# Performance work log

Measured on AMD Instinct MI355X. Metric: run time of the kernel, lower is better.

The kernel has to match this reference:

```python
import jax, jax.numpy as jnp
import numpy as np

VOCAB, EMB, HID, KSZ, VSZ = 10000, 512, 1024, 128, 128
N, T_ENC, T_DEC = 64, 500, 200


def lstm_cell(x, h, c, W_ih, W_hh, b_ih, b_hh):
    # PyTorch LSTMCell gate order: i, f, g, o
    gates = x @ W_ih.T + b_ih + h @ W_hh.T + b_hh
    i, f, g, o = jnp.split(gates, 4, axis=-1)
    c_new = jax.nn.sigmoid(f) * c + jax.nn.sigmoid(i) * jnp.tanh(g)
    h_new = jax.nn.sigmoid(o) * jnp.tanh(c_new)
    return h_new, c_new


def setup_inputs() -> dict:
    key = jax.random.key(0)
    ks = jax.random.split(key, 16)
    s = 0.02
    emb_table = jax.random.normal(ks[0], (VOCAB, EMB), jnp.float32) * s
    emb_table = emb_table.at[0].set(0.0)  # padding_idx=0
    inp = {
        "key": jax.random.normal(ks[1], (N, T_ENC, KSZ), jnp.float32),
        "value": jax.random.normal(ks[2], (N, T_ENC, VSZ), jnp.float32),
        "src_lens": jax.random.randint(ks[3], (N,), 1, T_ENC + 1),
        "text": jax.random.randint(ks[4], (N, T_DEC), 0, VOCAB),
        "emb_table": emb_table,
        "W_ih1": jax.random.normal(ks[5], (4 * HID, EMB + VSZ), jnp.float32) * s,
        "W_hh1": jax.random.normal(ks[6], (4 * HID, HID), jnp.float32) * s,
        "b_ih1": jnp.zeros((4 * HID,), jnp.float32),
        "b_hh1": jnp.zeros((4 * HID,), jnp.float32),
        "W_ih2": jax.random.normal(ks[7], (4 * KSZ, HID), jnp.float32) * s,
        "W_hh2": jax.random.normal(ks[8], (4 * KSZ, KSZ), jnp.float32) * s,
        "b_ih2": jnp.zeros((4 * KSZ,), jnp.float32),
        "b_hh2": jnp.zeros((4 * KSZ,), jnp.float32),
        "W_out": jax.random.normal(ks[9], (VOCAB, KSZ + VSZ), jnp.float32) * s,
        "b_out": jnp.zeros((VOCAB,), jnp.float32),
    }
    return inp


def reference(key, value, src_lens, text, emb_table, W_ih1, W_hh1, b_ih1, b_hh1,
              W_ih2, W_hh2, b_ih2, b_hh2, W_out, b_out):
    n, t_enc = key.shape[0], key.shape[1]
    # attention mask over encoder steps: True where position >= src_len
    mask = jnp.arange(t_enc)[None, :] >= src_lens[:, None]  # (N, T_enc)
    embeddings = emb_table[text]  # (N, T_dec, EMB) teacher forcing

    def step(carry, x_emb):
        h1, c1, h2, c2 = carry
        # attention: query = h2 (output of 2nd LSTMCell)
        energy = jnp.einsum('ntk,nk->nt', key, h2)
        energy = jnp.where(mask, -1e9, energy)
        att = jax.nn.softmax(energy, axis=1)
        ctx = jnp.einsum('nt,ntv->nv', att, value)
        inp = jnp.concatenate([x_emb, ctx], axis=1)
        h1, c1 = lstm_cell(inp, h1, c1, W_ih1, W_hh1, b_ih1, b_hh1)
        h2, c2 = lstm_cell(h1, h2, c2, W_ih2, W_hh2, b_ih2, b_hh2)
        logits = jnp.concatenate([h2, ctx], axis=1) @ W_out.T + b_out
        return (h1, c1, h2, c2), logits

    init = (jnp.zeros((n, W_hh1.shape[1])), jnp.zeros((n, W_hh1.shape[1])),
            jnp.zeros((n, W_hh2.shape[1])), jnp.zeros((n, W_hh2.shape[1])))
    _, preds = jax.lax.scan(step, init, jnp.swapaxes(embeddings, 0, 1))
    return jnp.swapaxes(preds, 0, 1)  # (N, T_dec, VOCAB)
```

## Files before the change

kernel.cpp:

```cpp
#include <hip/hip_runtime.h>
#include <hip/hip_bf16.h>
#include <math.h>


#define NB    64
#define TENC  500
#define TDEC  200
#define EMBD  512
#define HID   1024
#define KSZ   128
#define VSZ   128
#define VOCAB 10000
#define K1    1664
#define K2    1152
#define NWG   256
#define NTH   512

typedef __bf16 bf16x8 __attribute__((ext_vector_type(8)));
typedef float f32x4 __attribute__((ext_vector_type(4)));
typedef unsigned long long u64;
#define MFMA16(a, b, c) __builtin_amdgcn_mfma_f32_16x16x32_bf16((a), (b), (c), 0, 0, 0)

constexpr size_t OFF_BAR   = 0;
constexpr size_t OFF_BS1   = 4096;
constexpr size_t OFF_BS2   = 20480;
constexpr size_t OFF_W2    = 22528;
constexpr size_t OFF_H2C   = 1202176;
constexpr size_t OFF_W1    = 7755776;
constexpr size_t OFF_WOUT  = 21387264;
constexpr size_t OFF_XEMB  = 26507264;
constexpr size_t OFF_H1R   = 39614464;
constexpr size_t OFF_CTXR  = 65959936;
constexpr size_t BIG_END   = 69253120;
constexpr size_t OFF_KEYBF = 69253120;
constexpr size_t OFF_VALBF = 77445120;
constexpr size_t KV_END    = 85637120;

__device__ __forceinline__ float sigm(float x) { return 1.0f / (1.0f + __expf(-x)); }
__device__ __forceinline__ float ftanh(float x) {
  float ax = fabsf(x);
  float e = __expf(2.0f * ax);
  float tv = 1.0f - 2.0f / (e + 1.0f);
  return copysignf(tv, x);
}
__device__ __forceinline__ float bf2f(unsigned u) { return __uint_as_float(u << 16); }
__device__ __forceinline__ bf16x8 ldfrag(const __hip_bfloat16* p) {
  return *reinterpret_cast<const bf16x8*>(p);
}
__device__ __forceinline__ bf16x8 ldfrag_nt(const __hip_bfloat16* p) {
  union { u64 u[2]; bf16x8 v; } r;
  r.u[0] = __builtin_nontemporal_load((const u64*)p);
  r.u[1] = __builtin_nontemporal_load((const u64*)(p + 4));
  return r.v;
}
__device__ __forceinline__ void st_u32_sys(void* p, unsigned v) {
  __hip_atomic_store((unsigned*)p, v, __ATOMIC_RELAXED, __HIP_MEMORY_SCOPE_AGENT);
}
__device__ __forceinline__ void st_u16_sys(void* p, unsigned short v) {
  __hip_atomic_store((unsigned short*)p, v, __ATOMIC_RELAXED, __HIP_MEMORY_SCOPE_AGENT);
}
__device__ __forceinline__ unsigned ld_u32_sys(const void* p) {
  return __hip_atomic_load((const unsigned*)p, __ATOMIC_RELAXED, __HIP_MEMORY_SCOPE_AGENT);
}
__device__ __forceinline__ unsigned pack2bf(float a, float b) {
  __hip_bfloat16 ha = __float2bfloat16(a), hb = __float2bfloat16(b);
  unsigned short ua = *(unsigned short*)&ha, ub = *(unsigned short*)&hb;
  return (unsigned)ua | ((unsigned)ub << 16);
}
__device__ __forceinline__ unsigned short f2bfu(float x) {
  __hip_bfloat16 h = __float2bfloat16(x);
  return *(unsigned short*)&h;
}

__global__ __launch_bounds__(256) void k_prep_w1(const float* __restrict__ Wih1,
                                                 const float* __restrict__ Whh1,
                                                 const float* __restrict__ bih1,
                                                 const float* __restrict__ bhh1,
                                                 __hip_bfloat16* __restrict__ W1bf,
                                                 float* __restrict__ bsum1) {
  int r = blockIdx.x;
  const float* wi = Wih1 + (size_t)r * 640;
  const float* wh = Whh1 + (size_t)r * 1024;
  for (int k = threadIdx.x; k < K1; k += 256)
    W1bf[(size_t)r * K1 + k] = __float2bfloat16(k < 640 ? wi[k] : wh[k - 640]);
  if (threadIdx.x == 0) bsum1[r] = bih1[r] + bhh1[r];
}

__global__ __launch_bounds__(256) void k_prep_w2(const float* __restrict__ Wih2,
                                                 const float* __restrict__ Whh2,
                                                 const float* __restrict__ bih2,
                                                 const float* __restrict__ bhh2,
                                                 __hip_bfloat16* __restrict__ W2bf,
                                                 float* __restrict__ bsum2) {
  int r = blockIdx.x;
  for (int k = threadIdx.x; k < K2; k += 256)
    W2bf[(size_t)r * K2 + k] =
        __float2bfloat16(k < 1024 ? Wih2[(size_t)r * 1024 + k]
                                  : Whh2[(size_t)r * 128 + k - 1024]);
  if (threadIdx.x == 0) bsum2[r] = bih2[r] + bhh2[r];
}

__global__ __launch_bounds__(256) void k_prep_wout(const float* __restrict__ Wout,
                                                   __hip_bfloat16* __restrict__ Woutbf) {
  int r0 = blockIdx.x * 16;
  for (int idx = threadIdx.x; idx < 16 * 256; idx += 256) {
    int r = r0 + (idx >> 8), k = idx & 255;
    Woutbf[(size_t)r * 256 + k] = __float2bfloat16(Wout[(size_t)r * 256 + k]);
  }
}

__global__ __launch_bounds__(256) void k_gather(const int* __restrict__ text,
                                                const float* __restrict__ emb,
                                                __hip_bfloat16* __restrict__ xembbf) {
  int t = blockIdx.x;
  __shared__ int tok[NB];
  if (threadIdx.x < NB) tok[threadIdx.x] = text[threadIdx.x * TDEC + t];
  __syncthreads();
  for (int idx = threadIdx.x; idx < NB * EMBD; idx += 256) {
    int n = idx >> 9, k = idx & 511;
    xembbf[((size_t)t * NB + n) * EMBD + k] =
        __float2bfloat16(emb[(size_t)tok[n] * EMBD + k]);
  }
}

__global__ __launch_bounds__(256) void k_prep_kv(const float* __restrict__ key,
                                                 const float* __restrict__ value,
                                                 __hip_bfloat16* __restrict__ keybf,
                                                 __hip_bfloat16* __restrict__ valbf) {
  int gsz = gridDim.x * 256;
  for (size_t i = blockIdx.x * 256 + threadIdx.x; i < (size_t)NB * TENC * KSZ; i += gsz) {
    keybf[i] = __float2bfloat16(key[i]);
    valbf[i] = __float2bfloat16(value[i]);
  }
}

__device__ __forceinline__ void gbar(unsigned* cnt, int ep, int wg, bool inv) {
  asm volatile("s_waitcnt vmcnt(0)" ::: "memory");
  __syncthreads();
  int tid = threadIdx.x;
  if (tid == 0) {
    if (inv)
      __hip_atomic_fetch_add(&cnt[(wg & 7) << 4], 1u, __ATOMIC_ACQ_REL,
                             __HIP_MEMORY_SCOPE_AGENT);
    else
      __hip_atomic_fetch_add(&cnt[(wg & 7) << 4], 1u, __ATOMIC_RELAXED,
                             __HIP_MEMORY_SCOPE_AGENT);
  }
  if (tid < 64) {
    unsigned need = (unsigned)ep * 16u;
    for (;;) {
      unsigned v = __hip_atomic_load(&cnt[(tid & 7) << 4], __ATOMIC_RELAXED,
                                     __HIP_MEMORY_SCOPE_AGENT);
      if (__all((int)(v >= need))) break;
      __builtin_amdgcn_s_sleep(1);
    }
    if (inv) {
      unsigned vv = __hip_atomic_load(&cnt[(tid & 7) << 4], __ATOMIC_ACQUIRE,
                                      __HIP_MEMORY_SCOPE_AGENT);
      (void)vv;
    }
  }
  __syncthreads();
}

struct LA {
  const float* key;
  const float* value;
  const int* slen;
  const __hip_bfloat16* keybf;
  const __hip_bfloat16* valbf;
  int kv;
  int big;
  const __hip_bfloat16* W1bf;
  const __hip_bfloat16* W2bf;
  const __hip_bfloat16* Woutbf;
  const __hip_bfloat16* xembbf;
  const float* bsum1;
  const float* bsum2;
  const float* bout;
  float* out;
  __hip_bfloat16* h1r;
  __hip_bfloat16* ctxr;
  __hip_bfloat16* h2cbf;
  __hip_bfloat16* pbuf;
  unsigned* ms;
  unsigned* flags;
  unsigned* bar_cnt;
};

__global__ __launch_bounds__(NTH) void k_loop(LA a) {
  const int wg = blockIdx.x, tid = threadIdx.x;

  __shared__ float bs1l[8][4];
  __shared__ unsigned short stmp[512];
  __shared__ __align__(16) char smem[33792];
  float* part = (float*)smem;
  float* gl   = (float*)(smem + 8192);
  float* partL = (float*)smem;
  float* glL   = (float*)(smem + 4096);
  float* h2s  = (float*)smem;
  float* e_l  = (float*)(smem + 2048);
  float* red  = (float*)(smem + 4096);
  float* ctxp = (float*)(smem + 6144);

  if (wg >= 128) {
    int o0 = wg - 128;
    int lane = tid & 63, w4 = tid >> 6;
    int ln15 = lane & 15, lg = lane >> 4, ko = lg * 8;
    for (int t = 0; t < TDEC; ++t) {
      if (tid < 64) {
        unsigned need = (3u * (unsigned)t + 3u) * 16u;
        for (;;) {
          unsigned v = __hip_atomic_load(&a.bar_cnt[(tid & 7) << 4],
                                         __ATOMIC_RELAXED, __HIP_MEMORY_SCOPE_AGENT);
          if (__all((int)(v >= need))) break;
          __builtin_amdgcn_s_sleep(8);
        }
      }
      __syncthreads();
      if (w4 < 4) {
        const __hip_bfloat16* ap =
            a.h2cbf + ((size_t)t * NB + w4 * 16 + ln15) * 256;
        bf16x8 afr[8];
        #pragma unroll
        for (int kk = 0; kk < 8; ++kk) afr[kk] = ldfrag(ap + kk * 32 + ko);
        for (int sub = 0; sub < 2; ++sub) {
          int o = o0 + sub * 128;
          if (o >= 157) break;
          int c0 = o * 64;
          #pragma unroll
          for (int s = 0; s < 4; ++s) {
            int c = c0 + s * 16 + ln15;
            bool ok = c < VOCAB;
            const __hip_bfloat16* bp = a.Woutbf + (size_t)c * 256;
            f32x4 acc = {0.f, 0.f, 0.f, 0.f};
            #pragma unroll
            for (int kk = 0; kk < 8; ++kk) {
              bf16x8 bv = ok ? ldfrag_nt(bp + kk * 32 + ko) : bf16x8{};
              acc = MFMA16(afr[kk], bv, acc);
            }
            if (ok) {
              float bb = a.bout[c];
              #pragma unroll
              for (int reg = 0; reg < 4; ++reg) {
                int nrow = w4 * 16 + 4 * lg + reg;
                __builtin_nontemporal_store(
                    acc[reg] + bb, &a.out[((size_t)nrow * TDEC + t) * VOCAB + c]);
              }
            }
          }
        }
      }
    }
    return;
  }

  const int lane = tid & 63, wid = tid >> 6;
  const int ln15 = lane & 15, lg = lane >> 4, ko = lg * 8;
  const int bg = wid & 3, kh = wid >> 2;
  const int d0 = wg * 8;
  const bool inv = (a.big == 0);
  const bool isMain = (wg < 64);
  const int n = wg & 63;
  const int len = a.slen[n];

  float creg0 = 0.f;
  float creg2 = 0.f;

  const __hip_bfloat16 *wb0, *wb1;
  {
    int g = ln15 & 3, s = ln15 >> 2;
    wb0 = a.W1bf + (size_t)(g * 1024 + d0 + 0 + s) * K1;
    wb1 = a.W1bf + (size_t)(g * 1024 + d0 + 4 + s) * K1;
  }
  const __hip_bfloat16* w2p = a.W2bf + (size_t)((ln15 & 3) * 128 + wg) * K2;
  const int nA = bg * 16 + ln15;

  if (tid < 32) bs1l[tid >> 2][tid & 3] = a.bsum1[(tid & 3) * 1024 + d0 + (tid >> 2)];
  if (isMain) {
    int v = tid & 127, ph = tid >> 7;
    float acc = 0.f;
    if (a.kv) {
      const unsigned short* vb = (const unsigned short*)a.valbf;
      for (int p = ph; p < len; p += 4)
        acc += bf2f(vb[((size_t)n * TENC + p) * VSZ + v]);
    } else {
      for (int p = ph; p < len; p += 4)
        acc += a.value[((size_t)n * TENC + p) * VSZ + v];
    }
    ctxp[ph * 128 + v] = acc;
    __syncthreads();
    if (tid < 64) {
      int vp = tid;
      float invl = 1.f / (float)len;
      float c0 = (ctxp[0 * 128 + 2 * vp] + ctxp[1 * 128 + 2 * vp] +
                  ctxp[2 * 128 + 2 * vp] + ctxp[3 * 128 + 2 * vp]) * invl;
      float c1 = (ctxp[0 * 128 + 2 * vp + 1] + ctxp[1 * 128 + 2 * vp + 1] +
                  ctxp[2 * 128 + 2 * vp + 1] + ctxp[3 * 128 + 2 * vp + 1]) * invl;
      unsigned pk = pack2bf(c0, c1);
      st_u32_sys(a.ctxr + (size_t)n * 128 + 2 * vp, pk);
      st_u32_sys(&a.h2cbf[((size_t)0 * NB + n) * 256 + 128 + 2 * vp], pk);
    }
  }
  int ep = 0;
  gbar(a.bar_cnt, ++ep, wg, inv);

  for (int t = 0; t < TDEC; ++t) {
    const __hip_bfloat16 *h1c, *ctxc;
    __hip_bfloat16 *h1n, *ctxn;
    if (a.big) {
      h1c = a.h1r + (size_t)t * 65536;
      h1n = a.h1r + (size_t)(t + 1) * 65536;
      ctxc = a.ctxr + (size_t)t * 8192;
      ctxn = a.ctxr + (size_t)(t + 1) * 8192;
    } else {
      h1c = a.h1r + (size_t)(t & 1) * 65536;
      h1n = a.h1r + (size_t)((t + 1) & 1) * 65536;
      ctxc = a.ctxr;
      ctxn = a.ctxr;
    }

    {
      const __hip_bfloat16* ax = a.xembbf + ((size_t)t * NB + nA) * EMBD;
      const __hip_bfloat16* ac = ctxc + nA * 128;
      const __hip_bfloat16* ah = h1c + nA * 1024;
      f32x4 q0 = {0, 0, 0, 0}, q1 = {0, 0, 0, 0};
      if (kh == 0) {
        #pragma unroll
        for (int s = 0; s < 16; ++s) {
          bf16x8 av = ldfrag(ax + s * 32 + ko);
          int o = s * 32 + ko;
          q0 = MFMA16(av, ldfrag(wb0 + o), q0);
          q1 = MFMA16(av, ldfrag(wb1 + o), q1);
        }
        #pragma unroll
        for (int s = 0; s < 4; ++s) {
          bf16x8 av = ldfrag(ac + s * 32 + ko);
          int o = 512 + s * 32 + ko;
          q0 = MFMA16(av, ldfrag(wb0 + o), q0);
          q1 = MFMA16(av, ldfrag(wb1 + o), q1);
        }
        #pragma unroll
        for (int s = 0; s < 6; ++s) {
          bf16x8 av = ldfrag(ah + s * 32 + ko);
          int o = 640 + s * 32 + ko;
          q0 = MFMA16(av, ldfrag(wb0 + o), q0);
          q1 = MFMA16(av, ldfrag(wb1 + o), q1);
        }
      } else {
        #pragma unroll
        for (int s = 0; s < 26; ++s) {
          bf16x8 av = ldfrag(ah + 192 + s * 32 + ko);
          int o = 832 + s * 32 + ko;
          q0 = MFMA16(av, ldfrag(wb0 + o), q0);
          q1 = MFMA16(av, ldfrag(wb1 + o), q1);
        }
      }
      if (kh == 1) {
        *(f32x4*)&part[(((bg * 2 + 0) * 64) + lane) * 4] = q0;
        *(f32x4*)&part[(((bg * 2 + 1) * 64) + lane) * 4] = q1;
      }
      __syncthreads();
      if (kh == 0) {
        q0 += *(f32x4*)&part[(((bg * 2 + 0) * 64) + lane) * 4];
        q1 += *(f32x4*)&part[(((bg * 2 + 1) * 64) + lane) * 4];
        #pragma unroll
        for (int r = 0; r < 4; ++r) {
          gl[((bg * 2 + 0) * 16 + (lg * 4 + r)) * 16 + ln15] = q0[r];
          gl[((bg * 2 + 1) * 16 + (lg * 4 + r)) * 16 + ln15] = q1[r];
        }
      }
      __syncthreads();
      {
        int nn = tid >> 3, dp = tid & 7;
        int bgg = nn >> 4, ii = nn & 15;
        int f = dp >> 2, s = dp & 3;
        float4 gA = *(float4*)&gl[(((bgg * 2 + f) * 16) + ii) * 16 + s * 4];
        float I = sigm(gA.x + bs1l[dp][0]);
        float F = sigm(gA.y + bs1l[dp][1]);
        float G = ftanh(gA.z + bs1l[dp][2]);
        float O = sigm(gA.w + bs1l[dp][3]);
        float cv = F * creg0 + I * G;
        creg0 = cv;
        stmp[nn * 8 + dp] = f2bfu(O * ftanh(cv));
      }
      __syncthreads();
      if (tid < 256) {
        int n3 = tid >> 2, e = tid & 3;
        unsigned pk = (unsigned)stmp[n3 * 8 + e * 2] |
                      ((unsigned)stmp[n3 * 8 + e * 2 + 1] << 16);
        st_u32_sys(h1n + n3 * 1024 + d0 + e * 2, pk);
      }
    }
    gbar(a.bar_cnt, ++ep, wg, inv);

    {
      const __hip_bfloat16* ah = h1n + nA * 1024;
      f32x4 q = {0.f, 0.f, 0.f, 0.f};
      if (kh == 0) {
        #pragma unroll
        for (int s = 0; s < 18; ++s)
          q = MFMA16(ldfrag(ah + s * 32 + ko), ldfrag(w2p + s * 32 + ko), q);
      } else {
        #pragma unroll
        for (int s = 0; s < 14; ++s)
          q = MFMA16(ldfrag(ah + 576 + s * 32 + ko), ldfrag(w2p + 576 + s * 32 + ko), q);
        if (t > 0) {
          const __hip_bfloat16* hp = a.h2cbf + ((size_t)(t - 1) * NB + nA) * 256;
          #pragma unroll
          for (int s = 0; s < 4; ++s)
            q = MFMA16(ldfrag(hp + s * 32 + ko), ldfrag(w2p + 1024 + s * 32 + ko), q);
        }
      }
      if (kh == 1) *(f32x4*)&partL[(bg * 64 + lane) * 4] = q;
      __syncthreads();
      if (kh == 0) {
        q += *(f32x4*)&partL[(bg * 64 + lane) * 4];
        #pragma unroll
        for (int r = 0; r < 4; ++r)
          glL[(bg * 16 + lg * 4 + r) * 16 + ln15] = q[r];
      }
      __syncthreads();
      if (tid < 64) {
        int n2 = tid;
        float4 g4 = *(float4*)&glL[n2 * 16];
        float I = sigm(g4.x + a.bsum2[wg]);
        float F = sigm(g4.y + a.bsum2[128 + wg]);
        float G = ftanh(g4.z + a.bsum2[256 + wg]);
        float O = sigm(g4.w + a.bsum2[384 + wg]);
        float cv = F * creg2 + I * G;
        creg2 = cv;
        st_u16_sys((unsigned short*)a.h2cbf + ((size_t)t * NB + n2) * 256 + wg,
                   f2bfu(O * ftanh(cv)));
      }
    }
    gbar(a.bar_cnt, ++ep, wg, inv);

    if (t < TDEC - 1) {
      if (tid < 64) {
        unsigned u = *(const unsigned*)((const unsigned short*)a.h2cbf +
                                        ((size_t)t * NB + n) * 256 + 2 * tid);
        h2s[2 * tid] = bf2f(u & 0xffffu);
        h2s[2 * tid + 1] = bf2f(u >> 16);
      }
      __syncthreads();
      const int base = isMain ? 0 : 250;
      const int lim = isMain ? (a.big ? (len < 250 ? len : 250) : len) : len;
      int p = base + tid;
      float e = -1e30f;
      if (tid < 250 + (isMain ? 6 : 0) && p < lim) {
        float s = 0.f;
        if (a.kv) {
          const uint4* kr = (const uint4*)(a.keybf + ((size_t)n * TENC + p) * KSZ);
          #pragma unroll
          for (int kk = 0; kk < 16; ++kk) {
            uint4 u = kr[kk];
            const float* hh = &h2s[kk * 8];
            s += bf2f(u.x & 0xffffu) * hh[0] + bf2f(u.x >> 16) * hh[1]
               + bf2f(u.y & 0xffffu) * hh[2] + bf2f(u.y >> 16) * hh[3]
               + bf2f(u.z & 0xffffu) * hh[4] + bf2f(u.z >> 16) * hh[5]
               + bf2f(u.w & 0xffffu) * hh[6] + bf2f(u.w >> 16) * hh[7];
          }
        } else {
          const float4* kr = (const float4*)(a.key + ((size_t)n * TENC + p) * KSZ);
          #pragma unroll 8
          for (int kk = 0; kk < 32; ++kk) {
            float4 u = kr[kk];
            const float* hh = &h2s[kk * 4];
            s += u.x * hh[0] + u.y * hh[1] + u.z * hh[2] + u.w * hh[3];
          }
        }
        e = s;
      }
      red[tid] = e;
      __syncthreads();
      for (int s2 = 256; s2 > 0; s2 >>= 1) {
        if (tid < s2) red[tid] = fmaxf(red[tid], red[tid + s2]);
        __syncthreads();
      }
      float mA = red[0];
      __syncthreads();
      bool act = (tid < 250 + (isMain ? 6 : 0)) && (base + tid < lim);
      float ex = act ? __expf(e - mA) : 0.f;
      e_l[tid] = ex;
      red[tid] = ex;
      __syncthreads();
      for (int s2 = 256; s2 > 0; s2 >>= 1) {
        if (tid < s2) red[tid] += red[tid + s2];
        __syncthreads();
      }
      float SA = red[0];
      {
        int w = tid >> 6, ln = tid & 63;
        float a0 = 0.f, a1 = 0.f;
        if (a.kv) {
          const unsigned short* vb = (const unsigned short*)a.valbf;
          for (int p2 = base + w; p2 < lim; p2 += 8) {
            unsigned u = *(const unsigned*)(vb + ((size_t)n * TENC + p2) * VSZ + 2 * ln);
            float ew = e_l[p2 - base];
            a0 += ew * bf2f(u & 0xffffu);
            a1 += ew * bf2f(u >> 16);
          }
        } else {
          for (int p2 = base + w; p2 < lim; p2 += 8) {
            float2 vv = *(const float2*)(a.value + ((size_t)n * TENC + p2) * VSZ + 2 * ln);
            float ew = e_l[p2 - base];
            a0 += ew * vv.x;
            a1 += ew * vv.y;
          }
        }
        ctxp[w * 128 + 2 * ln] = a0;
        ctxp[w * 128 + 2 * ln + 1] = a1;
      }
      __syncthreads();
      if (!isMain) {
        if (tid < 64) {
          int vp = tid;
          float p0 = 0.f, p1 = 0.f;
          #pragma unroll
          for (int w2 = 0; w2 < 8; ++w2) {
            p0 += ctxp[w2 * 128 + 2 * vp];
            p1 += ctxp[w2 * 128 + 2 * vp + 1];
          }
          st_u32_sys(a.pbuf + n * 128 + 2 * vp, pack2bf(p0, p1));
        }
        if (tid == 0) {
          st_u32_sys(a.ms + n * 2, __float_as_uint(mA));
          st_u32_sys(a.ms + n * 2 + 1, __float_as_uint(SA));
        }
        asm volatile("s_waitcnt vmcnt(0)" ::: "memory");
        __syncthreads();
        if (tid == 0) st_u32_sys(&a.flags[n], (unsigned)(t + 1));
      } else {
        if (a.big && tid == 0) {
          while (__hip_atomic_load(&a.flags[n], __ATOMIC_RELAXED,
                                   __HIP_MEMORY_SCOPE_AGENT) < (unsigned)(t + 1))
            __builtin_amdgcn_s_sleep(2);
        }
        __syncthreads();
        if (tid < 64) {
          int vp = tid;
          float PA0 = 0.f, PA1 = 0.f;
          #pragma unroll
          for (int w2 = 0; w2 < 8; ++w2) {
            PA0 += ctxp[w2 * 128 + 2 * vp];
            PA1 += ctxp[w2 * 128 + 2 * vp + 1];
          }
          float c0, c1;
          if (a.big) {
            float mB = __uint_as_float(ld_u32_sys(a.ms + n * 2));
            float SB = __uint_as_float(ld_u32_sys(a.ms + n * 2 + 1));
            unsigned pbu = ld_u32_sys(a.pbuf + n * 128 + 2 * vp);
            float m2 = fmaxf(mA, mB);
            float fA = __expf(mA - m2), fB = __expf(mB - m2);
            float ivs = 1.f / (SA * fA + SB * fB);
            c0 = (PA0 * fA + bf2f(pbu & 0xffffu) * fB) * ivs;
            c1 = (PA1 * fA + bf2f(pbu >> 16) * fB) * ivs;
          } else {
            float ivs = 1.f / SA;
            c0 = PA0 * ivs;
            c1 = PA1 * ivs;
          }
          unsigned pk = pack2bf(c0, c1);
          st_u32_sys(ctxn + (size_t)n * 128 + 2 * vp, pk);
          st_u32_sys(&a.h2cbf[((size_t)(t + 1) * NB + n) * 256 + 128 + 2 * vp], pk);
        }
      }
    }
    gbar(a.bar_cnt, ++ep, wg, inv);
  }
}

extern "C" void kernel_launch(void* const* d_in, const int* in_sizes, int n_in,
                              void* d_out, int out_size, void* d_ws, size_t ws_size,
                              hipStream_t stream) {
  (void)in_sizes; (void)n_in; (void)out_size;
  const float* key   = (const float*)d_in[0];
  const float* value = (const float*)d_in[1];
  const int*   slen  = (const int*)d_in[2];
  const int*   text  = (const int*)d_in[3];
  const float* emb   = (const float*)d_in[4];
  const float* Wih1  = (const float*)d_in[5];
  const float* Whh1  = (const float*)d_in[6];
  const float* bih1  = (const float*)d_in[7];
  const float* bhh1  = (const float*)d_in[8];
  const float* Wih2  = (const float*)d_in[9];
  const float* Whh2  = (const float*)d_in[10];
  const float* bih2  = (const float*)d_in[11];
  const float* bhh2  = (const float*)d_in[12];
  const float* Wout  = (const float*)d_in[13];
  const float* bout  = (const float*)d_in[14];
  float* out = (float*)d_out;
  char* ws = (char*)d_ws;

  int big = (ws_size >= BIG_END) ? 1 : 0;
  int kv  = (ws_size >= KV_END) ? 1 : 0;

  __hip_bfloat16* W1bf   = (__hip_bfloat16*)(ws + OFF_W1);
  __hip_bfloat16* W2bf   = (__hip_bfloat16*)(ws + OFF_W2);
  __hip_bfloat16* Woutbf = (__hip_bfloat16*)(ws + OFF_WOUT);
  __hip_bfloat16* xembbf = (__hip_bfloat16*)(ws + OFF_XEMB);
  __hip_bfloat16* h2cbf  = (__hip_bfloat16*)(ws + OFF_H2C);
  float* bsum1 = (float*)(ws + OFF_BS1);
  float* bsum2 = (float*)(ws + OFF_BS2);
  __hip_bfloat16* keybf = (__hip_bfloat16*)(ws + OFF_KEYBF);
  __hip_bfloat16* valbf = (__hip_bfloat16*)(ws + OFF_VALBF);

  hipMemsetAsync(ws, 0, 4096, stream);
  hipMemsetAsync(ws + OFF_H1R, 0, 262144, stream);
  k_prep_w1<<<4096, 256, 0, stream>>>(Wih1, Whh1, bih1, bhh1, W1bf, bsum1);
  k_prep_w2<<<512, 256, 0, stream>>>(Wih2, Whh2, bih2, bhh2, W2bf, bsum2);
  k_prep_wout<<<625, 256, 0, stream>>>(Wout, Woutbf);
  k_gather<<<TDEC, 256, 0, stream>>>(text, emb, xembbf);
  if (kv) k_prep_kv<<<2048, 256, 0, stream>>>(key, value, keybf, valbf);

  LA la;
  la.key = key; la.value = value; la.slen = slen;
  la.keybf = keybf; la.valbf = valbf; la.kv = kv; la.big = big;
  la.W1bf = W1bf; la.W2bf = W2bf; la.Woutbf = Woutbf; la.xembbf = xembbf;
  la.bsum1 = bsum1; la.bsum2 = bsum2; la.bout = bout; la.out = out;
  la.h1r = (__hip_bfloat16*)(ws + OFF_H1R);
  la.ctxr = (__hip_bfloat16*)(ws + OFF_CTXR);
  la.h2cbf = h2cbf;
  la.pbuf = (__hip_bfloat16*)(ws + OFF_CTXR) + (size_t)200 * 8192;
  la.ms = (unsigned*)(ws + 2048);
  la.flags = (unsigned*)(ws + 2560);
  la.bar_cnt = (unsigned*)(ws + OFF_BAR);

  void* args[] = {&la};
  hipLaunchCooperativeKernel((void*)k_loop, dim3(NWG), dim3(NTH), args, 0, stream);
}
```

Measured before the change: 9.366 ms.

## Fuse LSTM2 into per-batch attention workgroups and drop a grid barrier

Moves the second LSTM cell out of a grid-distributed MFMA stage. Each of the 64 main workgroups now computes all 512 gates for its own batch row, using a transposed bf16 W2 and scalar dot products, and keeps h2/c2 in shared memory. This removes one grid-wide barrier per decoder step. The helper workgroups that handle the second half of the attention now wait on a per-row flag instead. In exchange, every main workgroup re-reads the full W2 matrix each step and does the gate math without tensor cores.

```diff
diff --git a/kernel.cpp b/kernel.cpp
--- a/kernel.cpp
+++ b/kernel.cpp
@@ -86,17 +86,19 @@
   if (threadIdx.x == 0) bsum1[r] = bih1[r] + bhh1[r];
 }
 
-__global__ __launch_bounds__(256) void k_prep_w2(const float* __restrict__ Wih2,
-                                                 const float* __restrict__ Whh2,
-                                                 const float* __restrict__ bih2,
-                                                 const float* __restrict__ bhh2,
-                                                 __hip_bfloat16* __restrict__ W2bf,
-                                                 float* __restrict__ bsum2) {
+__global__ __launch_bounds__(256) void k_prep_w2t(const float* __restrict__ Wih2,
+                                                  const float* __restrict__ Whh2,
+                                                  const float* __restrict__ bih2,
+                                                  const float* __restrict__ bhh2,
+                                                  __hip_bfloat16* __restrict__ W2T,
+                                                  float* __restrict__ bsum2) {
   int r = blockIdx.x;
-  for (int k = threadIdx.x; k < K2; k += 256)
-    W2bf[(size_t)r * K2 + k] =
-        __float2bfloat16(k < 1024 ? Wih2[(size_t)r * 1024 + k]
-                                  : Whh2[(size_t)r * 128 + k - 1024]);
+  for (int idx = threadIdx.x; idx < K2; idx += 256) {
+    int kb = idx >> 3, j = idx & 7;
+    float v = (idx < 1024) ? Wih2[(size_t)r * 1024 + idx]
+                           : Whh2[(size_t)r * 128 + idx - 1024];
+    W2T[((size_t)(kb * 512 + r)) * 8 + j] = __float2bfloat16(v);
+  }
   if (threadIdx.x == 0) bsum2[r] = bih2[r] + bhh2[r];
 }
 
@@ -172,7 +174,7 @@
   int kv;
   int big;
   const __hip_bfloat16* W1bf;
-  const __hip_bfloat16* W2bf;
+  const __hip_bfloat16* W2T;
   const __hip_bfloat16* Woutbf;
   const __hip_bfloat16* xembbf;
   const float* bsum1;
@@ -184,7 +186,8 @@
   __hip_bfloat16* h2cbf;
   __hip_bfloat16* pbuf;
   unsigned* ms;
-  unsigned* flags;
+  unsigned* pflag;
+  unsigned* hflag;
   unsigned* bar_cnt;
 };
 
@@ -193,15 +196,17 @@
 
   __shared__ float bs1l[8][4];
   __shared__ unsigned short stmp[512];
+  __shared__ float h2st[128];
+  __shared__ float c2st[128];
   __shared__ __align__(16) char smem[33792];
   float* part = (float*)smem;
   float* gl   = (float*)(smem + 8192);
-  float* partL = (float*)smem;
-  float* glL   = (float*)(smem + 4096);
-  float* h2s  = (float*)smem;
-  float* e_l  = (float*)(smem + 2048);
-  float* red  = (float*)(smem + 4096);
-  float* ctxp = (float*)(smem + 6144);
+  float* h1s  = (float*)smem;
+  float* g2   = (float*)(smem + 4096);
+  float* e_l  = (float*)(smem + 6144);
+  float* red  = (float*)(smem + 8192);
+  float* ctxp = (float*)(smem + 10240);
+  float* h2s  = (float*)(smem + 14336);
 
   if (wg >= 128) {
     int o0 = wg - 128;
@@ -209,7 +214,7 @@
     int ln15 = lane & 15, lg = lane >> 4, ko = lg * 8;
     for (int t = 0; t < TDEC; ++t) {
       if (tid < 64) {
-        unsigned need = (3u * (unsigned)t + 3u) * 16u;
+        unsigned need = (2u * (unsigned)t + 3u) * 16u;
         for (;;) {
           unsigned v = __hip_atomic_load(&a.bar_cnt[(tid & 7) << 4],
                                          __ATOMIC_RELAXED, __HIP_MEMORY_SCOPE_AGENT);
@@ -265,7 +270,6 @@
   const int len = a.slen[n];
 
   float creg0 = 0.f;
-  float creg2 = 0.f;
 
   const __hip_bfloat16 *wb0, *wb1;
   {
@@ -273,10 +277,10 @@
     wb0 = a.W1bf + (size_t)(g * 1024 + d0 + 0 + s) * K1;
     wb1 = a.W1bf + (size_t)(g * 1024 + d0 + 4 + s) * K1;
   }
-  const __hip_bfloat16* w2p = a.W2bf + (size_t)((ln15 & 3) * 128 + wg) * K2;
   const int nA = bg * 16 + ln15;
 
   if (tid < 32) bs1l[tid >> 2][tid & 3] = a.bsum1[(tid & 3) * 1024 + d0 + (tid >> 2)];
+  if (tid < 128) { h2st[tid] = 0.f; c2st[tid] = 0.f; }
   if (isMain) {
     int v = tid & 127, ph = tid >> 7;
     float acc = 0.f;
@@ -394,146 +398,115 @@
     }
     gbar(a.bar_cnt, ++ep, wg, inv);
 
-    {
-      const __hip_bfloat16* ah = h1n + nA * 1024;
-      f32x4 q = {0.f, 0.f, 0.f, 0.f};
-      if (kh == 0) {
-        #pragma unroll
-        for (int s = 0; s < 18; ++s)
-          q = MFMA16(ldfrag(ah + s * 32 + ko), ldfrag(w2p + s * 32 + ko), q);
-      } else {
-        #pragma unroll
-        for (int s = 0; s < 14; ++s)
-          q = MFMA16(ldfrag(ah + 576 + s * 32 + ko), ldfrag(w2p + 576 + s * 32 + ko), q);
-        if (t > 0) {
-          const __hip_bfloat16* hp = a.h2cbf + ((size_t)(t - 1) * NB + nA) * 256;
-          #pragma unroll
-          for (int s = 0; s < 4; ++s)
-            q = MFMA16(ldfrag(hp + s * 32 + ko), ldfrag(w2p + 1024 + s * 32 + ko), q);
-        }
-      }
-      if (kh == 1) *(f32x4*)&partL[(bg * 64 + lane) * 4] = q;
-      __syncthreads();
-      if (kh == 0) {
-        q += *(f32x4*)&partL[(bg * 64 + lane) * 4];
-        #pragma unroll
-        for (int r = 0; r < 4; ++r)
-          glL[(bg * 16 + lg * 4 + r) * 16 + ln15] = q[r];
-      }
-      __syncthreads();
-      if (tid < 64) {
-        int n2 = tid;
-        float4 g4 = *(float4*)&glL[n2 * 16];
-        float I = sigm(g4.x + a.bsum2[wg]);
-        float F = sigm(g4.y + a.bsum2[128 + wg]);
-        float G = ftanh(g4.z + a.bsum2[256 + wg]);
-        float O = sigm(g4.w + a.bsum2[384 + wg]);
-        float cv = F * creg2 + I * G;
-        creg2 = cv;
-        st_u16_sys((unsigned short*)a.h2cbf + ((size_t)t * NB + n2) * 256 + wg,
-                   f2bfu(O * ftanh(cv)));
-      }
-    }
-    gbar(a.bar_cnt, ++ep, wg, inv);
-
-    if (t < TDEC - 1) {
-      if (tid < 64) {
-        unsigned u = *(const unsigned*)((const unsigned short*)a.h2cbf +
-                                        ((size_t)t * NB + n) * 256 + 2 * tid);
-        h2s[2 * tid] = bf2f(u & 0xffffu);
-        h2s[2 * tid + 1] = bf2f(u >> 16);
-      }
-      __syncthreads();
-      const int base = isMain ? 0 : 250;
-      const int lim = isMain ? (a.big ? (len < 250 ? len : 250) : len) : len;
-      int p = base + tid;
-      float e = -1e30f;
-      if (tid < 250 + (isMain ? 6 : 0) && p < lim) {
-        float s = 0.f;
-        if (a.kv) {
-          const uint4* kr = (const uint4*)(a.keybf + ((size_t)n * TENC + p) * KSZ);
-          #pragma unroll
-          for (int kk = 0; kk < 16; ++kk) {
-            uint4 u = kr[kk];
-            const float* hh = &h2s[kk * 8];
-            s += bf2f(u.x & 0xffffu) * hh[0] + bf2f(u.x >> 16) * hh[1]
-               + bf2f(u.y & 0xffffu) * hh[2] + bf2f(u.y >> 16) * hh[3]
-               + bf2f(u.z & 0xffffu) * hh[4] + bf2f(u.z >> 16) * hh[5]
-               + bf2f(u.w & 0xffffu) * hh[6] + bf2f(u.w >> 16) * hh[7];
-          }
-        } else {
-          const float4* kr = (const float4*)(a.key + ((size_t)n * TENC + p) * KSZ);
-          #pragma unroll 8
-          for (int kk = 0; kk < 32; ++kk) {
-            float4 u = kr[kk];
-            const float* hh = &h2s[kk * 4];
-            s += u.x * hh[0] + u.y * hh[1] + u.z * hh[2] + u.w * hh[3];
-          }
-        }
-        e = s;
-      }
-      red[tid] = e;
-      __syncthreads();
-      for (int s2 = 256; s2 > 0; s2 >>= 1) {
-        if (tid < s2) red[tid] = fmaxf(red[tid], red[tid + s2]);
+    if (isMain) {
+      if (tid < 256) {
+        u64 u = *(const u64*)(h1n + (size_t)n * 1024 + tid * 4);
+        h1s[tid * 4 + 0] = bf2f((unsigned)(u & 0xffffu));
+        h1s[tid * 4 + 1] = bf2f((unsigned)((u >> 16) & 0xffffu));
+        h1s[tid * 4 + 2] = bf2f((unsigned)((u >> 32) & 0xffffu));
+        h1s[tid * 4 + 3] = bf2f((unsigned)(u >> 48));
+      }
+      __syncthreads();
+      {
+        float accg = 0.f;
+        #pragma unroll 8
+        for (int kb = 0; kb < 144; ++kb) {
+          uint4 wv = *(const uint4*)(a.W2T + ((size_t)kb * 512 + tid) * 8);
+          const float* in = (kb < 128) ? &h1s[kb * 8] : &h2st[(kb - 128) * 8];
+          accg += bf2f(wv.x & 0xffffu) * in[0] + bf2f(wv.x >> 16) * in[1]
+                + bf2f(wv.y & 0xffffu) * in[2] + bf2f(wv.y >> 16) * in[3]
+                + bf2f(wv.z & 0xffffu) * in[4] + bf2f(wv.z >> 16) * in[5]
+                + bf2f(wv.w & 0xffffu) * in[6] + bf2f(wv.w >> 16) * in[7];
+        }
+        g2[tid] = accg;
+      }
+      __syncthreads();
+      if (tid < 128) {
+        int d = tid;
+        float I = sigm(g2[d] + a.bsum2[d]);
+        float F = sigm(g2[128 + d] + a.bsum2[128 + d]);
+        float G = ftanh(g2[256 + d] + a.bsum2[256 + d]);
+        float O = sigm(g2[384 + d] + a.bsum2[384 + d]);
+        float cv = F * c2st[d] + I * G;
+        c2st[d] = cv;
+        float h = O * ftanh(cv);
+        h2st[d] = h;
+        st_u16_sys((unsigned short*)a.h2cbf + ((size_t)t * NB + n) * 256 + d,
+                   f2bfu(h));
+      }
+      asm volatile("s_waitcnt vmcnt(0)" ::: "memory");
+      __syncthreads();
+      if (tid == 0) st_u32_sys(&a.hflag[n], (unsigned)(t + 1));
+
+      if (t < TDEC - 1) {
+        const int lim = a.big ? (len < 250 ? len : 250) : len;
+        float e = -1e30f;
+        if (tid < 256 && tid < lim) {
+          float s = 0.f;
+          if (a.kv) {
+            const uint4* kr = (const uint4*)(a.keybf + ((size_t)n * TENC + tid) * KSZ);
+            #pragma unroll
+            for (int kk = 0; kk < 16; ++kk) {
+              uint4 u = kr[kk];
+              const float* hh = &h2st[kk * 8];
+              s += bf2f(u.x & 0xffffu) * hh[0] + bf2f(u.x >> 16) * hh[1]
+                 + bf2f(u.y & 0xffffu) * hh[2] + bf2f(u.y >> 16) * hh[3]
+                 + bf2f(u.z & 0xffffu) * hh[4] + bf2f(u.z >> 16) * hh[5]
+                 + bf2f(u.w & 0xffffu) * hh[6] + bf2f(u.w >> 16) * hh[7];
+            }
+          } else {
+            const float4* kr = (const float4*)(a.key + ((size_t)n * TENC + tid) * KSZ);
+            #pragma unroll 8
+            for (int kk = 0; kk < 32; ++kk) {
+              float4 u = kr[kk];
+              const float* hh = &h2st[kk * 4];
+              s += u.x * hh[0] + u.y * hh[1] + u.z * hh[2] + u.w * hh[3];
+            }
+          }
+          e = s;
+        }
+        red[tid] = e;
         __syncthreads();
-      }
-      float mA = red[0];
-      __syncthreads();
-      bool act = (tid < 250 + (isMain ? 6 : 0)) && (base + tid < lim);
-      float ex = act ? __expf(e - mA) : 0.f;
-      e_l[tid] = ex;
-      red[tid] = ex;
-      __syncthreads();
-      for (int s2 = 256; s2 > 0; s2 >>= 1) {
-        if (tid < s2) red[tid] += red[tid + s2];
+        for (int s2 = 256; s2 > 0; s2 >>= 1) {
+          if (tid < s2) red[tid] = fmaxf(red[tid], red[tid + s2]);
+          __syncthreads();
+        }
+        float mA = red[0];
         __syncthreads();
-      }
-      float SA = red[0];
-      {
-        int w = tid >> 6, ln = tid & 63;
-        float a0 = 0.f, a1 = 0.f;
-        if (a.kv) {
-          const unsigned short* vb = (const unsigned short*)a.valbf;
-          for (int p2 = base + w; p2 < lim; p2 += 8) {
-            unsigned u = *(const unsigned*)(vb + ((size_t)n * TENC + p2) * VSZ + 2 * ln);
-            float ew = e_l[p2 - base];
-            a0 += ew * bf2f(u & 0xffffu);
-            a1 += ew * bf2f(u >> 16);
-          }
-        } else {
-          for (int p2 = base + w; p2 < lim; p2 += 8) {
-            float2 vv = *(const float2*)(a.value + ((size_t)n * TENC + p2) * VSZ + 2 * ln);
-            float ew = e_l[p2 - base];
-            a0 += ew * vv.x;
-            a1 += ew * vv.y;
-          }
-        }
-        ctxp[w * 128 + 2 * ln] = a0;
-        ctxp[w * 128 + 2 * ln + 1] = a1;
-      }
-      __syncthreads();
-      if (!isMain) {
-        if (tid < 64) {
-          int vp = tid;
-          float p0 = 0.f, p1 = 0.f;
-          #pragma unroll
-          for (int w2 = 0; w2 < 8; ++w2) {
-            p0 += ctxp[w2 * 128 + 2 * vp];
-            p1 += ctxp[w2 * 128 + 2 * vp + 1];
-          }
-          st_u32_sys(a.pbuf + n * 128 + 2 * vp, pack2bf(p0, p1));
-        }
-        if (tid == 0) {
-          st_u32_sys(a.ms + n * 2, __float_as_uint(mA));
-          st_u32_sys(a.ms + n * 2 + 1, __float_as_uint(SA));
-        }
-        asm volatile("s_waitcnt vmcnt(0)" ::: "memory");
+        float ex = (tid < 256 && tid < lim) ? __expf(e - mA) : 0.f;
+        e_l[tid] = ex;
+        red[tid] = ex;
         __syncthreads();
-        if (tid == 0) st_u32_sys(&a.flags[n], (unsigned)(t + 1));
-      } else {
+        for (int s2 = 256; s2 > 0; s2 >>= 1) {
+          if (tid < s2) red[tid] += red[tid + s2];
+          __syncthreads();
+        }
+        float SA = red[0];
+        {
+          int w = tid >> 6, ln = tid & 63;
+          float a0 = 0.f, a1 = 0.f;
+          if (a.kv) {
+            const unsigned short* vb = (const unsigned short*)a.valbf;
+            for (int p2 = w; p2 < lim; p2 += 8) {
+              unsigned u = *(const unsigned*)(vb + ((size_t)n * TENC + p2) * VSZ + 2 * ln);
+              float ew = e_l[p2];
+              a0 += ew * bf2f(u & 0xffffu);
+              a1 += ew * bf2f(u >> 16);
+            }
+          } else {
+            for (int p2 = w; p2 < lim; p2 += 8) {
+              float2 vv = *(const float2*)(a.value + ((size_t)n * TENC + p2) * VSZ + 2 * ln);
+              float ew = e_l[p2];
+              a0 += ew * vv.x;
+              a1 += ew * vv.y;
+            }
+          }
+          ctxp[w * 128 + 2 * ln] = a0;
+          ctxp[w * 128 + 2 * ln + 1] = a1;
+        }
+        __syncthreads();
         if (a.big && tid == 0) {
-          while (__hip_atomic_load(&a.flags[n], __ATOMIC_RELAXED,
+          while (__hip_atomic_load(&a.pflag[n], __ATOMIC_RELAXED,
                                    __HIP_MEMORY_SCOPE_AGENT) < (unsigned)(t + 1))
             __builtin_amdgcn_s_sleep(2);
         }
@@ -566,6 +539,103 @@
           st_u32_sys(&a.h2cbf[((size_t)(t + 1) * NB + n) * 256 + 128 + 2 * vp], pk);
         }
       }
+    } else if (a.big && t < TDEC - 1) {
+      if (tid == 0) {
+        while (__hip_atomic_load(&a.hflag[n], __ATOMIC_RELAXED,
+                                 __HIP_MEMORY_SCOPE_AGENT) < (unsigned)(t + 1))
+          __builtin_amdgcn_s_sleep(2);
+      }
+      __syncthreads();
+      if (tid < 64) {
+        unsigned u = *(const unsigned*)((const unsigned short*)a.h2cbf +
+                                        ((size_t)t * NB + n) * 256 + 2 * tid);
+        h2s[2 * tid] = bf2f(u & 0xffffu);
+        h2s[2 * tid + 1] = bf2f(u >> 16);
+      }
+      __syncthreads();
+      int p = 250 + tid;
+      float e = -1e30f;
+      if (tid < 250 && p < len) {
+        float s = 0.f;
+        if (a.kv) {
+          const uint4* kr = (const uint4*)(a.keybf + ((size_t)n * TENC + p) * KSZ);
+          #pragma unroll
+          for (int kk = 0; kk < 16; ++kk) {
+            uint4 u = kr[kk];
+            const float* hh = &h2s[kk * 8];
+            s += bf2f(u.x & 0xffffu) * hh[0] + bf2f(u.x >> 16) * hh[1]
+               + bf2f(u.y & 0xffffu) * hh[2] + bf2f(u.y >> 16) * hh[3]
+               + bf2f(u.z & 0xffffu) * hh[4] + bf2f(u.z >> 16) * hh[5]
+               + bf2f(u.w & 0xffffu) * hh[6] + bf2f(u.w >> 16) * hh[7];
+          }
+        } else {
+          const float4* kr = (const float4*)(a.key + ((size_t)n * TENC + p) * KSZ);
+          #pragma unroll 8
+          for (int kk = 0; kk < 32; ++kk) {
+            float4 u = kr[kk];
+            const float* hh = &h2s[kk * 4];
+            s += u.x * hh[0] + u.y * hh[1] + u.z * hh[2] + u.w * hh[3];
+          }
+        }
+        e = s;
+      }
+      red[tid] = e;
+      __syncthreads();
+      for (int s2 = 256; s2 > 0; s2 >>= 1) {
+        if (tid < s2) red[tid] = fmaxf(red[tid], red[tid + s2]);
+        __syncthreads();
+      }
+      float mB = red[0];
+      __syncthreads();
+      float ex = (tid < 250 && p < len) ? __expf(e - mB) : 0.f;
+      e_l[tid] = ex;
+      red[tid] = ex;
+      __syncthreads();
+      for (int s2 = 256; s2 > 0; s2 >>= 1) {
+        if (tid < s2) red[tid] += red[tid + s2];
+        __syncthreads();
+      }
+      float SB = red[0];
+      {
+        int w = tid >> 6, ln = tid & 63;
+        float a0 = 0.f, a1 = 0.f;
+        if (a.kv) {
+          const unsigned short* vb = (const unsigned short*)a.valbf;
+          for (int p2 = 250 + w; p2 < len; p2 += 8) {
+            unsigned u = *(const unsigned*)(vb + ((size_t)n * TENC + p2) * VSZ + 2 * ln);
+            float ew = e_l[p2 - 250];
+            a0 += ew * bf2f(u & 0xffffu);
+            a1 += ew * bf2f(u >> 16);
+          }
+        } else {
+          for (int p2 = 250 + w; p2 < len; p2 += 8) {
+            float2 vv = *(const float2*)(a.value + ((size_t)n * TENC + p2) * VSZ + 2 * ln);
+            float ew = e_l[p2 - 250];
+            a0 += ew * vv.x;
+            a1 += ew * vv.y;
+          }
+        }
+        ctxp[w * 128 + 2 * ln] = a0;
+        ctxp[w * 128 + 2 * ln + 1] = a1;
+      }
+      __syncthreads();
+      if (tid < 64) {
+        int vp = tid;
+        float p0 = 0.f, p1 = 0.f;
+        #pragma unroll
+        for (int w2 = 0; w2 < 8; ++w2) {
+          p0 += ctxp[w2 * 128 + 2 * vp];
+          p1 += ctxp[w2 * 128 + 2 * vp + 1];
+        }
+        st_u32_sys(a.pbuf + n * 128 + 2 * vp, pack2bf(p0, p1));
+      }
+      if (tid == 0) {
+        st_u32_sys(a.ms + n * 2, __float_as_uint(mB));
+        st_u32_sys(a.ms + n * 2 + 1, __float_as_uint(SB));
+      }
+      asm volatile("s_waitcnt vmcnt(0)" ::: "memory");
+      __syncthreads();
+      if (tid == 0) st_u32_sys(&a.pflag[n], (unsigned)(t + 1));
     }
     gbar(a.bar_cnt, ++ep, wg, inv);
   }
@@ -597,7 +667,7 @@
   int kv  = (ws_size >= KV_END) ? 1 : 0;
 
   __hip_bfloat16* W1bf   = (__hip_bfloat16*)(ws + OFF_W1);
-  __hip_bfloat16* W2bf   = (__hip_bfloat16*)(ws + OFF_W2);
+  __hip_bfloat16* W2T    = (__hip_bfloat16*)(ws + OFF_W2);
   __hip_bfloat16* Woutbf = (__hip_bfloat16*)(ws + OFF_WOUT);
   __hip_bfloat16* xembbf = (__hip_bfloat16*)(ws + OFF_XEMB);
   __hip_bfloat16* h2cbf  = (__hip_bfloat16*)(ws + OFF_H2C);
@@ -609,7 +679,7 @@
   hipMemsetAsync(ws, 0, 4096, stream);
   hipMemsetAsync(ws + OFF_H1R, 0, 262144, stream);
   k_prep_w1<<<4096, 256, 0, stream>>>(Wih1, Whh1, bih1, bhh1, W1bf, bsum1);
-  k_prep_w2<<<512, 256, 0, stream>>>(Wih2, Whh2, bih2, bhh2, W2bf, bsum2);
+  k_prep_w2t<<<512, 256, 0, stream>>>(Wih2, Whh2, bih2, bhh2, W2T, bsum2);
   k_prep_wout<<<625, 256, 0, stream>>>(Wout, Woutbf);
   k_gather<<<TDEC, 256, 0, stream>>>(text, emb, xembbf);
   if (kv) k_prep_kv<<<2048, 256, 0, stream>>>(key, value, keybf, valbf);
@@ -617,14 +687,15 @@
   LA la;
   la.key = key; la.value = value; la.slen = slen;
   la.keybf = keybf; la.valbf = valbf; la.kv = kv; la.big = big;
-  la.W1bf = W1bf; la.W2bf = W2bf; la.Woutbf = Woutbf; la.xembbf = xembbf;
+  la.W1bf = W1bf; la.W2T = W2T; la.Woutbf = Woutbf; la.xembbf = xembbf;
   la.bsum1 = bsum1; la.bsum2 = bsum2; la.bout = bout; la.out = out;
   la.h1r = (__hip_bfloat16*)(ws + OFF_H1R);
   la.ctxr = (__hip_bfloat16*)(ws + OFF_CTXR);
   la.h2cbf = h2cbf;
   la.pbuf = (__hip_bfloat16*)(ws + OFF_CTXR) + (size_t)200 * 8192;
   la.ms = (unsigned*)(ws + 2048);
-  la.flags = (unsigned*)(ws + 2560);
+  la.pflag = (unsigned*)(ws + 2560);
+  la.hflag = (unsigned*)(ws + 3072);
   la.bar_cnt = (unsigned*)(ws + OFF_BAR);
 
   void* args[] = {&la};
```

After: 15.26 ms. +63.0%, slower.
